# Kernel optimization log

Hardware: AMD Instinct MI355X
Metric: run time of the kernel (lower is better)

## Reference

```python
import jax, jax.numpy as jnp
import numpy as np

N_NODES = 100000
N_EDGES = 1600000
N_FEAT = 128
HIDDEN = 128
N_GRAPHS = 100


def setup_inputs() -> dict:
    key = jax.random.key(0)
    ks = jax.random.split(key, 12)
    glorot = lambda k, fi, fo: jax.random.normal(k, (fo, fi), jnp.float32) * (1.0 / np.sqrt(fi))
    x = jax.random.normal(ks[0], (N_NODES, N_FEAT), jnp.float32)
    edge_index = jax.random.randint(ks[1], (2, N_EDGES), 0, N_NODES, jnp.int64)
    batch = jnp.sort(jax.random.randint(ks[2], (N_NODES,), 0, N_GRAPHS, jnp.int64))
    return {
        "x": x,
        "edge_index": edge_index,
        "batch": batch,
        "W1": glorot(ks[3], N_FEAT, HIDDEN), "b1": jnp.zeros((HIDDEN,), jnp.float32),
        "W2": glorot(ks[4], HIDDEN, HIDDEN), "b2": jnp.zeros((HIDDEN,), jnp.float32),
        "W3": glorot(ks[5], HIDDEN, HIDDEN), "b3": jnp.zeros((HIDDEN,), jnp.float32),
        "W4": glorot(ks[6], HIDDEN, HIDDEN), "b4": jnp.zeros((HIDDEN,), jnp.float32),
    }


def _aggregate(x, edge_index):
    # GIN aggregation with eps=0: (1+eps)*x_i + sum_{j in N(i)} x_j
    src, dst = edge_index[0], edge_index[1]
    agg = jax.ops.segment_sum(x[src], dst, num_segments=N_NODES)
    return x + agg


def _mlp(h, Wa, ba, Wb, bb):
    h = jax.nn.relu(h @ Wa.T + ba)
    return jax.nn.relu(h @ Wb.T + bb)


def reference(x, edge_index, batch, W1, b1, W2, b2, W3, b3, W4, b4):
    # conv1: GINConv(MLP1), then extra relu (no-op after MLP's relu), dropout in eval = identity
    h = _mlp(_aggregate(x, edge_index), W1, b1, W2, b2)
    # conv2: GINConv(MLP2), then relu
    h = _mlp(_aggregate(h, edge_index), W3, b3, W4, b4)
    # global mean pool over graphs
    sums = jax.ops.segment_sum(h, batch, num_segments=N_GRAPHS)
    counts = jax.ops.segment_sum(jnp.ones((h.shape[0],), h.dtype), batch, num_segments=N_GRAPHS)
    x_pool = sums / jnp.maximum(counts, 1.0)[:, None]
    return (x_pool, h)
```

## Files before the change

### kernel.cpp

```cpp
#include <hip/hip_runtime.h>

#define N_NODES  100000
#define N_EDGES  1600000
#define NF       128
#define N_GRAPHS 100
#define NBKT     196
#define BKT_SHIFT 9
#define EPB      4096
#define EB_GRID  391

typedef __attribute__((ext_vector_type(8))) short bf16x8;
typedef __attribute__((ext_vector_type(4))) float f32x4;
typedef unsigned int uint32;

__device__ __forceinline__ unsigned short f2bf(float f) {
    union { float f; uint32 u; } x; x.f = f;
    return (unsigned short)((x.u + 0x7fffu + ((x.u >> 16) & 1u)) >> 16);
}
__device__ __forceinline__ uint32 pack2bf(float a, float b) {
    union { float f; uint32 u; } x, y; x.f = a; y.f = b;
    uint32 lo = (x.u + 0x7fffu + ((x.u >> 16) & 1u)) >> 16;
    uint32 hi = (y.u + 0x7fffu + ((y.u >> 16) & 1u)) & 0xffff0000u;
    return lo | hi;
}

__global__ __launch_bounds__(256) void conv_bf16(const float4* __restrict__ in,
                                                 uint4* __restrict__ out, int n8) {
    int i = blockIdx.x * 256 + threadIdx.x;
    if (i >= n8) return;
    float4 a = in[i * 2], b = in[i * 2 + 1];
    uint4 o;
    o.x = pack2bf(a.x, a.y); o.y = pack2bf(a.z, a.w);
    o.z = pack2bf(b.x, b.y); o.w = pack2bf(b.z, b.w);
    out[i] = o;
}

__global__ __launch_bounds__(256) void conv_w4(const float4* __restrict__ w1,
                                               const float4* __restrict__ w2,
                                               const float4* __restrict__ w3,
                                               const float4* __restrict__ w4,
                                               uint4* __restrict__ out) {
    int i = blockIdx.x * 256 + threadIdx.x;
    int wi = i >> 11, li = i & 2047;
    const float4* src = (wi == 0) ? w1 : (wi == 1) ? w2 : (wi == 2) ? w3 : w4;
    float4 a = src[li * 2], b = src[li * 2 + 1];
    uint4 o;
    o.x = pack2bf(a.x, a.y); o.y = pack2bf(a.z, a.w);
    o.z = pack2bf(b.x, b.y); o.w = pack2bf(b.z, b.w);
    out[i] = o;
}

__global__ __launch_bounds__(256) void bhist(const int* __restrict__ dst,
                                             int* __restrict__ gcnt) {
    __shared__ int h[NBKT];
    int t = threadIdx.x;
    if (t < NBKT) h[t] = 0;
    __syncthreads();
    int e0 = blockIdx.x * EPB;
    #pragma unroll
    for (int i = 0; i < 16; ++i) {
        int e = e0 + i * 256 + t;
        if (e < N_EDGES) atomicAdd(&h[dst[e] >> BKT_SHIFT], 1);
    }
    __syncthreads();
    if (t < NBKT) atomicAdd(&gcnt[t], h[t]);
}

__global__ __launch_bounds__(256) void bscan(const int* __restrict__ gcnt,
                                             int* __restrict__ bbase,
                                             int* __restrict__ cur,
                                             int* __restrict__ rowptr) {
    __shared__ int s[256];
    int t = threadIdx.x;
    int v = (t < NBKT) ? gcnt[t] : 0;
    s[t] = v;
    __syncthreads();
    for (int o = 1; o < 256; o <<= 1) {
        int x = (t >= o) ? s[t - o] : 0;
        __syncthreads();
        s[t] += x;
        __syncthreads();
    }
    if (t < NBKT) { int ex = s[t] - v; bbase[t] = ex; cur[t] = ex; }
    if (t == 0)  { bbase[NBKT] = N_EDGES; rowptr[N_NODES] = N_EDGES; }
}

__global__ __launch_bounds__(256) void bscatter(const int* __restrict__ src,
                                                const int* __restrict__ dst,
                                                int* __restrict__ cur,
                                                uint32* __restrict__ ebuf) {
    __shared__ int lh[NBKT], lbase[NBKT], lcur[NBKT];
    int t = threadIdx.x;
    if (t < NBKT) lh[t] = 0;
    __syncthreads();
    int e0 = blockIdx.x * EPB;
    int d[16];
    #pragma unroll
    for (int i = 0; i < 16; ++i) {
        int e = e0 + i * 256 + t;
        d[i] = -1;
        if (e < N_EDGES) { d[i] = dst[e]; atomicAdd(&lh[d[i] >> BKT_SHIFT], 1); }
    }
    __syncthreads();
    if (t < NBKT) { lbase[t] = atomicAdd(&cur[t], lh[t]); lcur[t] = 0; }
    __syncthreads();
    #pragma unroll
    for (int i = 0; i < 16; ++i) {
        int e = e0 + i * 256 + t;
        if (e < N_EDGES) {
            int b = d[i] >> BKT_SHIFT;
            int off = atomicAdd(&lcur[b], 1);
            ebuf[lbase[b] + off] = ((uint32)(d[i] & 511) << 17) | (uint32)src[e];
        }
    }
}

__global__ __launch_bounds__(256) void bfine(const uint32* __restrict__ ebuf,
                                             const int* __restrict__ bbase,
                                             int* __restrict__ rowptr,
                                             int* __restrict__ csr) {
    __shared__ int deg[512];
    __shared__ int off[512];
    __shared__ int sc[256];
    int t = threadIdx.x;
    int bkt = blockIdx.x;
    int beg = bbase[bkt], end = bbase[bkt + 1];
    deg[t] = 0; deg[t + 256] = 0;
    __syncthreads();
    for (int e = beg + t; e < end; e += 256)
        atomicAdd(&deg[ebuf[e] >> 17], 1);
    __syncthreads();
    int d0 = deg[2 * t], d1 = deg[2 * t + 1];
    sc[t] = d0 + d1;
    __syncthreads();
    for (int o = 1; o < 256; o <<= 1) {
        int x = (t >= o) ? sc[t - o] : 0;
        __syncthreads();
        sc[t] += x;
        __syncthreads();
    }
    int ex = sc[t] - (d0 + d1);
    off[2 * t] = ex; off[2 * t + 1] = ex + d0;
    __syncthreads();
    int node0 = bkt << BKT_SHIFT;
    for (int i = t; i < 512; i += 256) {
        int node = node0 + i;
        if (node < N_NODES) rowptr[node] = beg + off[i];
    }
    __syncthreads();
    for (int e = beg + t; e < end; e += 256) {
        uint32 u = ebuf[e];
        int dl = u >> 17, s = (int)(u & 0x1FFFFu);
        int pos = atomicAdd(&off[dl], 1);
        csr[beg + pos] = s;
    }
}

__global__ __launch_bounds__(256) void gather_agg_bf16(const uint4* __restrict__ x,
                                                       const int* __restrict__ rowptr,
                                                       const int* __restrict__ csr,
                                                       uint4* __restrict__ out) {
    int idx = blockIdx.x * 256 + threadIdx.x;
    int node = idx >> 4, c = idx & 15;
    int beg = rowptr[node], end = rowptr[node + 1];

    float acc[8];
    {
        uint4 v = x[node * 16 + c];
        uint32 u[4] = {v.x, v.y, v.z, v.w};
        #pragma unroll
        for (int i = 0; i < 4; ++i) {
            union { uint32 b; float f; } lo, hi;
            lo.b = u[i] << 16; hi.b = u[i] & 0xffff0000u;
            acc[2 * i] = lo.f; acc[2 * i + 1] = hi.f;
        }
    }
    for (int e = beg; e < end; ++e) {
        int s = csr[e];
        uint4 v = x[s * 16 + c];
        uint32 u[4] = {v.x, v.y, v.z, v.w};
        #pragma unroll
        for (int i = 0; i < 4; ++i) {
            union { uint32 b; float f; } lo, hi;
            lo.b = u[i] << 16; hi.b = u[i] & 0xffff0000u;
            acc[2 * i] += lo.f; acc[2 * i + 1] += hi.f;
        }
    }
    uint4 o;
    o.x = pack2bf(acc[0], acc[1]); o.y = pack2bf(acc[2], acc[3]);
    o.z = pack2bf(acc[4], acc[5]); o.w = pack2bf(acc[6], acc[7]);
    out[node * 16 + c] = o;
}

template <bool F32OUT>
__global__ __launch_bounds__(256) void mlp_mfma(const unsigned short* __restrict__ A,
                                                const unsigned short* __restrict__ Wa,
                                                const float* __restrict__ ba,
                                                const unsigned short* __restrict__ Wb,
                                                const float* __restrict__ bb,
                                                void* __restrict__ Cout, int M) {
    __shared__ unsigned short As[128 * 136];
    __shared__ unsigned short Ws[128 * 136];
    __shared__ float bs1[128], bs2[128];
    int tid  = threadIdx.x;
    int row0 = blockIdx.x * 128;

    #pragma unroll
    for (int it = 0; it < 8; ++it) {
        int li = it * 256 + tid;
        int r = li >> 4, s = li & 15;
        uint4 v = make_uint4(0u, 0u, 0u, 0u);
        if (row0 + r < M) v = *(const uint4*)(A + (size_t)(row0 + r) * NF + s * 8);
        *(uint4*)&As[r * 136 + s * 8] = v;
        *(uint4*)&Ws[r * 136 + s * 8] = *(const uint4*)(Wa + r * NF + s * 8);
    }
    if (tid < 128) { bs1[tid] = ba[tid]; bs2[tid] = bb[tid]; }
    __syncthreads();

    int wv = tid >> 6;
    int l  = tid & 63;
    int lm = l & 15;
    int q  = l >> 4;

    f32x4 acc[2][8];
    #pragma unroll
    for (int i = 0; i < 2; ++i)
        #pragma unroll
        for (int j = 0; j < 8; ++j) acc[i][j] = (f32x4){0.f, 0.f, 0.f, 0.f};

    #pragma unroll
    for (int ks = 0; ks < 4; ++ks) {
        int ko = ks * 32 + q * 8;
        bf16x8 a0 = *(const bf16x8*)&As[(wv * 32 + lm) * 136 + ko];
        bf16x8 a1 = *(const bf16x8*)&As[(wv * 32 + 16 + lm) * 136 + ko];
        #pragma unroll
        for (int ct = 0; ct < 8; ++ct) {
            bf16x8 b = *(const bf16x8*)&Ws[(ct * 16 + lm) * 136 + ko];
            acc[0][ct] = __builtin_amdgcn_mfma_f32_16x16x32_bf16(a0, b, acc[0][ct], 0, 0, 0);
            acc[1][ct] = __builtin_amdgcn_mfma_f32_16x16x32_bf16(a1, b, acc[1][ct], 0, 0, 0);
        }
    }
    __syncthreads();

    #pragma unroll
    for (int rt = 0; rt < 2; ++rt)
        #pragma unroll
        for (int ct = 0; ct < 8; ++ct) {
            int col = ct * 16 + lm;
            float bv = bs1[col];
            #pragma unroll
            for (int r = 0; r < 4; ++r) {
                int rr = wv * 32 + rt * 16 + q * 4 + r;
                As[rr * 136 + col] = f2bf(fmaxf(acc[rt][ct][r] + bv, 0.f));
            }
        }
    #pragma unroll
    for (int it = 0; it < 8; ++it) {
        int li = it * 256 + tid;
        int r = li >> 4, s = li & 15;
        *(uint4*)&Ws[r * 136 + s * 8] = *(const uint4*)(Wb + r * NF + s * 8);
    }
    __syncthreads();

    #pragma unroll
    for (int i = 0; i < 2; ++i)
        #pragma unroll
        for (int j = 0; j < 8; ++j) acc[i][j] = (f32x4){0.f, 0.f, 0.f, 0.f};

    #pragma unroll
    for (int ks = 0; ks < 4; ++ks) {
        int ko = ks * 32 + q * 8;
        bf16x8 a0 = *(const bf16x8*)&As[(wv * 32 + lm) * 136 + ko];
        bf16x8 a1 = *(const bf16x8*)&As[(wv * 32 + 16 + lm) * 136 + ko];
        #pragma unroll
        for (int ct = 0; ct < 8; ++ct) {
            bf16x8 b = *(const bf16x8*)&Ws[(ct * 16 + lm) * 136 + ko];
            acc[0][ct] = __builtin_amdgcn_mfma_f32_16x16x32_bf16(a0, b, acc[0][ct], 0, 0, 0);
            acc[1][ct] = __builtin_amdgcn_mfma_f32_16x16x32_bf16(a1, b, acc[1][ct], 0, 0, 0);
        }
    }

    #pragma unroll
    for (int rt = 0; rt < 2; ++rt)
        #pragma unroll
        for (int ct = 0; ct < 8; ++ct) {
            int col = ct * 16 + lm;
            float bv = bs2[col];
            #pragma unroll
            for (int r = 0; r < 4; ++r) {
                int row = row0 + wv * 32 + rt * 16 + q * 4 + r;
                if (row < M) {
                    float v = fmaxf(acc[rt][ct][r] + bv, 0.f);
                    if (F32OUT) ((float*)Cout)[(size_t)row * NF + col] = v;
                    else ((unsigned short*)Cout)[(size_t)row * NF + col] = f2bf(v);
                }
            }
        }
}

__global__ __launch_bounds__(256) void pool_sum2(const float* __restrict__ h,
                                                 const int* __restrict__ batch,
                                                 float* __restrict__ sums) {
    int t = threadIdx.x;
    int f = t & 127, seg = t >> 7;
    int n0 = blockIdx.x * 128 + seg * 64;
    if (n0 >= N_NODES) return;
    int n1 = min(n0 + 64, N_NODES);
    int cur = batch[n0];
    float acc = 0.f;
    for (int n = n0; n < n1; ++n) {
        int g = batch[n];
        if (g != cur) {
            atomicAdd(&sums[cur * NF + f], acc);
            acc = 0.f; cur = g;
        }
        acc += h[(size_t)n * NF + f];
    }
    atomicAdd(&sums[cur * NF + f], acc);
}

__global__ __launch_bounds__(256) void pool_div2(const float* __restrict__ sums,
                                                 const int* __restrict__ batch,
                                                 float* __restrict__ out) {
    int i = blockIdx.x * 256 + threadIdx.x;
    if (i >= N_GRAPHS * NF) return;
    int g = i >> 7;
    int lo = 0, hi = N_NODES;
    while (lo < hi) { int m = (lo + hi) >> 1; if (batch[m] < g) lo = m + 1; else hi = m; }
    int lo2 = lo, hi2 = N_NODES;
    while (lo2 < hi2) { int m = (lo2 + hi2) >> 1; if (batch[m] < g + 1) lo2 = m + 1; else hi2 = m; }
    float cnt = (float)(lo2 - lo);
    out[i] = sums[i] / fmaxf(cnt, 1.f);
}

extern "C" void kernel_launch(void* const* d_in, const int* in_sizes, int n_in,
                              void* d_out, int out_size, void* d_ws, size_t ws_size,
                              hipStream_t stream) {
    const float* x     = (const float*)d_in[0];
    const int*   ei    = (const int*)d_in[1];
    const int*   batch = (const int*)d_in[2];
    const float* W1 = (const float*)d_in[3];  const float* b1 = (const float*)d_in[4];
    const float* W2 = (const float*)d_in[5];  const float* b2 = (const float*)d_in[6];
    const float* W3 = (const float*)d_in[7];  const float* b3 = (const float*)d_in[8];
    const float* W4 = (const float*)d_in[9];  const float* b4 = (const float*)d_in[10];
    const int* src = ei;
    const int* dst = ei + N_EDGES;

    float* out   = (float*)d_out;
    float* h_out = out + N_GRAPHS * NF;

    const size_t NE = (size_t)N_NODES * NF;
    unsigned short* xb = (unsigned short*)d_ws;
    unsigned short* t0 = xb + NE;
    unsigned short* t1 = t0 + NE;
    unsigned short* Wb = t1 + NE;
    int*    rowptr = (int*)(Wb + 4 * NF * NF);
    int*    csr    = rowptr + N_NODES + 1;
    uint32* ebuf   = (uint32*)(csr + N_EDGES);
    int*    gcnt   = (int*)(ebuf + N_EDGES);
    int*    bbase  = gcnt + NBKT;
    int*    curp   = bbase + NBKT + 1;
    float*  sums   = (float*)(curp + NBKT);

    const int gather_blocks = N_NODES * 16 / 256;
    const int gemm_blocks   = (N_NODES + 127) / 128;

    hipMemsetAsync(gcnt, 0, NBKT * sizeof(int), stream);
    hipMemsetAsync(sums, 0, N_GRAPHS * NF * sizeof(float), stream);

    conv_bf16<<<(int)(NE / 8 + 255) / 256, 256, 0, stream>>>((const float4*)x, (uint4*)xb, (int)(NE / 8));
    conv_w4<<<32, 256, 0, stream>>>((const float4*)W1, (const float4*)W2,
                                    (const float4*)W3, (const float4*)W4, (uint4*)Wb);

    bhist<<<EB_GRID, 256, 0, stream>>>(dst, gcnt);
    bscan<<<1, 256, 0, stream>>>(gcnt, bbase, curp, rowptr);
    bscatter<<<EB_GRID, 256, 0, stream>>>(src, dst, curp, ebuf);
    bfine<<<NBKT, 256, 0, stream>>>(ebuf, bbase, rowptr, csr);

    gather_agg_bf16<<<gather_blocks, 256, 0, stream>>>((const uint4*)xb, rowptr, csr, (uint4*)t0);
    mlp_mfma<false><<<gemm_blocks, 256, 0, stream>>>(t0, Wb + 0 * NF * NF, b1,
                                                     Wb + 1 * NF * NF, b2, t1, N_NODES);

    gather_agg_bf16<<<gather_blocks, 256, 0, stream>>>((const uint4*)t1, rowptr, csr, (uint4*)t0);
    mlp_mfma<true ><<<gemm_blocks, 256, 0, stream>>>(t0, Wb + 2 * NF * NF, b3,
                                                     Wb + 3 * NF * NF, b4, h_out, N_NODES);

    pool_sum2<<<(N_NODES + 127) / 128, 256, 0, stream>>>(h_out, batch, sums);
    pool_div2<<<(N_GRAPHS * NF + 255) / 256, 256, 0, stream>>>(sums, batch, out);
}
```

Baseline: 428.4 us.

## Fuse prep kernels, use fixed-capacity buckets, and load MLP operands directly from global

One prep kernel now converts x and the weights to bf16 and zeroes the counters, replacing two memsets and two conversion launches. The histogram and scan passes are dropped by giving each destination bucket a fixed-capacity slot (CAP) and storing per-node row ends. bfine runs with 512 threads and a single-level scan. The MLP kernel reads A and W fragments straight from global memory instead of staging them in LDS, keeping LDS only for the intermediate activation, with a 4-block occupancy hint. The fixed capacity can overflow if a bucket gets more than CAP edges, and direct global loads may cost more memory traffic than the LDS staging did.

```diff
diff --git a/kernel.cpp b/kernel.cpp
--- a/kernel.cpp
+++ b/kernel.cpp
@@ -6,6 +6,7 @@
 #define N_GRAPHS 100
 #define NBKT     196
 #define BKT_SHIFT 9
+#define CAP      12288
 #define EPB      4096
 #define EB_GRID  391
 
@@ -24,72 +25,42 @@
     return lo | hi;
 }
 
-__global__ __launch_bounds__(256) void conv_bf16(const float4* __restrict__ in,
-                                                 uint4* __restrict__ out, int n8) {
-    int i = blockIdx.x * 256 + threadIdx.x;
-    if (i >= n8) return;
-    float4 a = in[i * 2], b = in[i * 2 + 1];
-    uint4 o;
-    o.x = pack2bf(a.x, a.y); o.y = pack2bf(a.z, a.w);
-    o.z = pack2bf(b.x, b.y); o.w = pack2bf(b.z, b.w);
-    out[i] = o;
-}
-
-__global__ __launch_bounds__(256) void conv_w4(const float4* __restrict__ w1,
-                                               const float4* __restrict__ w2,
-                                               const float4* __restrict__ w3,
-                                               const float4* __restrict__ w4,
-                                               uint4* __restrict__ out) {
-    int i = blockIdx.x * 256 + threadIdx.x;
-    int wi = i >> 11, li = i & 2047;
-    const float4* src = (wi == 0) ? w1 : (wi == 1) ? w2 : (wi == 2) ? w3 : w4;
-    float4 a = src[li * 2], b = src[li * 2 + 1];
-    uint4 o;
-    o.x = pack2bf(a.x, a.y); o.y = pack2bf(a.z, a.w);
-    o.z = pack2bf(b.x, b.y); o.w = pack2bf(b.z, b.w);
-    out[i] = o;
-}
-
-__global__ __launch_bounds__(256) void bhist(const int* __restrict__ dst,
-                                             int* __restrict__ gcnt) {
-    __shared__ int h[NBKT];
-    int t = threadIdx.x;
-    if (t < NBKT) h[t] = 0;
-    __syncthreads();
-    int e0 = blockIdx.x * EPB;
-    #pragma unroll
-    for (int i = 0; i < 16; ++i) {
-        int e = e0 + i * 256 + t;
-        if (e < N_EDGES) atomicAdd(&h[dst[e] >> BKT_SHIFT], 1);
-    }
-    __syncthreads();
-    if (t < NBKT) atomicAdd(&gcnt[t], h[t]);
-}
-
-__global__ __launch_bounds__(256) void bscan(const int* __restrict__ gcnt,
-                                             int* __restrict__ bbase,
-                                             int* __restrict__ cur,
-                                             int* __restrict__ rowptr) {
-    __shared__ int s[256];
-    int t = threadIdx.x;
-    int v = (t < NBKT) ? gcnt[t] : 0;
-    s[t] = v;
-    __syncthreads();
-    for (int o = 1; o < 256; o <<= 1) {
-        int x = (t >= o) ? s[t - o] : 0;
-        __syncthreads();
-        s[t] += x;
-        __syncthreads();
-    }
-    if (t < NBKT) { int ex = s[t] - v; bbase[t] = ex; cur[t] = ex; }
-    if (t == 0)  { bbase[NBKT] = N_EDGES; rowptr[N_NODES] = N_EDGES; }
+__global__ __launch_bounds__(256) void prep(const float4* __restrict__ x,
+                                            const float4* __restrict__ w1,
+                                            const float4* __restrict__ w2,
+                                            const float4* __restrict__ w3,
+                                            const float4* __restrict__ w4,
+                                            uint4* __restrict__ xb, uint4* __restrict__ wb,
+                                            int* __restrict__ cur, float* __restrict__ sums) {
+    int bid = blockIdx.x, t = threadIdx.x;
+    if (bid < 6250) {
+        int i = bid * 256 + t;
+        float4 a = x[i * 2], b = x[i * 2 + 1];
+        uint4 o;
+        o.x = pack2bf(a.x, a.y); o.y = pack2bf(a.z, a.w);
+        o.z = pack2bf(b.x, b.y); o.w = pack2bf(b.z, b.w);
+        xb[i] = o;
+    } else if (bid < 6282) {
+        int i = (bid - 6250) * 256 + t;
+        int wi = i >> 11, li = i & 2047;
+        const float4* s = (wi == 0) ? w1 : (wi == 1) ? w2 : (wi == 2) ? w3 : w4;
+        float4 a = s[li * 2], b = s[li * 2 + 1];
+        uint4 o;
+        o.x = pack2bf(a.x, a.y); o.y = pack2bf(a.z, a.w);
+        o.z = pack2bf(b.x, b.y); o.w = pack2bf(b.z, b.w);
+        wb[i] = o;
+    } else {
+        int idx = (bid - 6282) * 256 + t;
+        for (int i = idx; i < N_GRAPHS * NF; i += 4096) sums[i] = 0.f;
+        if (idx < NBKT) cur[idx] = 0;
+    }
 }
 
 __global__ __launch_bounds__(256) void bscatter(const int* __restrict__ src,
                                                 const int* __restrict__ dst,
                                                 int* __restrict__ cur,
                                                 uint32* __restrict__ ebuf) {
-    __shared__ int lh[NBKT], lbase[NBKT], lcur[NBKT];
+    __shared__ int lh[NBKT], lbase[NBKT];
     int t = threadIdx.x;
     if (t < NBKT) lh[t] = 0;
     __syncthreads();
@@ -102,67 +73,64 @@
         if (e < N_EDGES) { d[i] = dst[e]; atomicAdd(&lh[d[i] >> BKT_SHIFT], 1); }
     }
     __syncthreads();
-    if (t < NBKT) { lbase[t] = atomicAdd(&cur[t], lh[t]); lcur[t] = 0; }
+    if (t < NBKT) { lbase[t] = t * CAP + atomicAdd(&cur[t], lh[t]); lh[t] = 0; }
     __syncthreads();
     #pragma unroll
     for (int i = 0; i < 16; ++i) {
         int e = e0 + i * 256 + t;
         if (e < N_EDGES) {
             int b = d[i] >> BKT_SHIFT;
-            int off = atomicAdd(&lcur[b], 1);
+            int off = atomicAdd(&lh[b], 1);
             ebuf[lbase[b] + off] = ((uint32)(d[i] & 511) << 17) | (uint32)src[e];
         }
     }
 }
 
-__global__ __launch_bounds__(256) void bfine(const uint32* __restrict__ ebuf,
-                                             const int* __restrict__ bbase,
+__global__ __launch_bounds__(512) void bfine(const uint32* __restrict__ ebuf,
+                                             const int* __restrict__ cur,
                                              int* __restrict__ rowptr,
+                                             int* __restrict__ rowend,
                                              int* __restrict__ csr) {
-    __shared__ int deg[512];
-    __shared__ int off[512];
-    __shared__ int sc[256];
+    __shared__ int deg[512], off[512];
     int t = threadIdx.x;
     int bkt = blockIdx.x;
-    int beg = bbase[bkt], end = bbase[bkt + 1];
-    deg[t] = 0; deg[t + 256] = 0;
-    __syncthreads();
-    for (int e = beg + t; e < end; e += 256)
+    int beg = bkt * CAP;
+    int end = beg + cur[bkt];
+    deg[t] = 0;
+    __syncthreads();
+    for (int e = beg + t; e < end; e += 512)
         atomicAdd(&deg[ebuf[e] >> 17], 1);
     __syncthreads();
-    int d0 = deg[2 * t], d1 = deg[2 * t + 1];
-    sc[t] = d0 + d1;
-    __syncthreads();
-    for (int o = 1; o < 256; o <<= 1) {
-        int x = (t >= o) ? sc[t - o] : 0;
+    int d = deg[t];
+    off[t] = d;
+    __syncthreads();
+    for (int o = 1; o < 512; o <<= 1) {
+        int x = (t >= o) ? off[t - o] : 0;
         __syncthreads();
-        sc[t] += x;
+        off[t] += x;
         __syncthreads();
     }
-    int ex = sc[t] - (d0 + d1);
-    off[2 * t] = ex; off[2 * t + 1] = ex + d0;
-    __syncthreads();
-    int node0 = bkt << BKT_SHIFT;
-    for (int i = t; i < 512; i += 256) {
-        int node = node0 + i;
-        if (node < N_NODES) rowptr[node] = beg + off[i];
-    }
-    __syncthreads();
-    for (int e = beg + t; e < end; e += 256) {
+    int ex = off[t] - d;
+    int node = (bkt << BKT_SHIFT) + t;
+    if (node < N_NODES) { rowptr[node] = beg + ex; rowend[node] = beg + ex + d; }
+    __syncthreads();
+    off[t] = ex;
+    __syncthreads();
+    for (int e = beg + t; e < end; e += 512) {
         uint32 u = ebuf[e];
-        int dl = u >> 17, s = (int)(u & 0x1FFFFu);
-        int pos = atomicAdd(&off[dl], 1);
-        csr[beg + pos] = s;
+        int pos = atomicAdd(&off[u >> 17], 1);
+        csr[beg + pos] = (int)(u & 0x1FFFFu);
     }
 }
 
 __global__ __launch_bounds__(256) void gather_agg_bf16(const uint4* __restrict__ x,
                                                        const int* __restrict__ rowptr,
+                                                       const int* __restrict__ rowend,
                                                        const int* __restrict__ csr,
                                                        uint4* __restrict__ out) {
     int idx = blockIdx.x * 256 + threadIdx.x;
     int node = idx >> 4, c = idx & 15;
-    int beg = rowptr[node], end = rowptr[node + 1];
+    int beg = rowptr[node], end = rowend[node];
 
     float acc[8];
     {
@@ -193,34 +161,21 @@
 }
 
 template <bool F32OUT>
-__global__ __launch_bounds__(256) void mlp_mfma(const unsigned short* __restrict__ A,
-                                                const unsigned short* __restrict__ Wa,
-                                                const float* __restrict__ ba,
-                                                const unsigned short* __restrict__ Wb,
-                                                const float* __restrict__ bb,
-                                                void* __restrict__ Cout, int M) {
-    __shared__ unsigned short As[128 * 136];
-    __shared__ unsigned short Ws[128 * 136];
-    __shared__ float bs1[128], bs2[128];
+__global__ __launch_bounds__(256, 4) void mlp_mfma(const unsigned short* __restrict__ A,
+                                                   const unsigned short* __restrict__ Wa,
+                                                   const float* __restrict__ ba,
+                                                   const unsigned short* __restrict__ Wb,
+                                                   const float* __restrict__ bb,
+                                                   void* __restrict__ Cout, int M) {
+    __shared__ unsigned short Mid[128 * 136];
     int tid  = threadIdx.x;
     int row0 = blockIdx.x * 128;
-
-    #pragma unroll
-    for (int it = 0; it < 8; ++it) {
-        int li = it * 256 + tid;
-        int r = li >> 4, s = li & 15;
-        uint4 v = make_uint4(0u, 0u, 0u, 0u);
-        if (row0 + r < M) v = *(const uint4*)(A + (size_t)(row0 + r) * NF + s * 8);
-        *(uint4*)&As[r * 136 + s * 8] = v;
-        *(uint4*)&Ws[r * 136 + s * 8] = *(const uint4*)(Wa + r * NF + s * 8);
-    }
-    if (tid < 128) { bs1[tid] = ba[tid]; bs2[tid] = bb[tid]; }
-    __syncthreads();
-
-    int wv = tid >> 6;
-    int l  = tid & 63;
-    int lm = l & 15;
-    int q  = l >> 4;
+    int wv = tid >> 6, l = tid & 63, lm = l & 15, q = l >> 4;
+
+    const unsigned short* pa0 = A + (size_t)min(row0 + wv * 32 + lm,      M - 1) * NF;
+    const unsigned short* pa1 = A + (size_t)min(row0 + wv * 32 + 16 + lm, M - 1) * NF;
+    const unsigned short* pwa = Wa + lm * NF;
+    const unsigned short* pwb = Wb + lm * NF;
 
     f32x4 acc[2][8];
     #pragma unroll
@@ -231,35 +186,28 @@
     #pragma unroll
     for (int ks = 0; ks < 4; ++ks) {
         int ko = ks * 32 + q * 8;
-        bf16x8 a0 = *(const bf16x8*)&As[(wv * 32 + lm) * 136 + ko];
-        bf16x8 a1 = *(const bf16x8*)&As[(wv * 32 + 16 + lm) * 136 + ko];
+        bf16x8 a0 = *(const bf16x8*)(pa0 + ko);
+        bf16x8 a1 = *(const bf16x8*)(pa1 + ko);
         #pragma unroll
         for (int ct = 0; ct < 8; ++ct) {
-            bf16x8 b = *(const bf16x8*)&Ws[(ct * 16 + lm) * 136 + ko];
+            bf16x8 b = *(const bf16x8*)(pwa + ct * 16 * NF + ko);
             acc[0][ct] = __builtin_amdgcn_mfma_f32_16x16x32_bf16(a0, b, acc[0][ct], 0, 0, 0);
             acc[1][ct] = __builtin_amdgcn_mfma_f32_16x16x32_bf16(a1, b, acc[1][ct], 0, 0, 0);
         }
     }
-    __syncthreads();
 
     #pragma unroll
     for (int rt = 0; rt < 2; ++rt)
         #pragma unroll
         for (int ct = 0; ct < 8; ++ct) {
             int col = ct * 16 + lm;
-            float bv = bs1[col];
+            float bv = ba[col];
             #pragma unroll
             for (int r = 0; r < 4; ++r) {
                 int rr = wv * 32 + rt * 16 + q * 4 + r;
-                As[rr * 136 + col] = f2bf(fmaxf(acc[rt][ct][r] + bv, 0.f));
+                Mid[rr * 136 + col] = f2bf(fmaxf(acc[rt][ct][r] + bv, 0.f));
             }
         }
-    #pragma unroll
-    for (int it = 0; it < 8; ++it) {
-        int li = it * 256 + tid;
-        int r = li >> 4, s = li & 15;
-        *(uint4*)&Ws[r * 136 + s * 8] = *(const uint4*)(Wb + r * NF + s * 8);
-    }
     __syncthreads();
 
     #pragma unroll
@@ -267,14 +215,16 @@
         #pragma unroll
         for (int j = 0; j < 8; ++j) acc[i][j] = (f32x4){0.f, 0.f, 0.f, 0.f};
 
+    const unsigned short* pm0 = &Mid[(wv * 32 + lm) * 136];
+    const unsigned short* pm1 = &Mid[(wv * 32 + 16 + lm) * 136];
     #pragma unroll
     for (int ks = 0; ks < 4; ++ks) {
         int ko = ks * 32 + q * 8;
-        bf16x8 a0 = *(const bf16x8*)&As[(wv * 32 + lm) * 136 + ko];
-        bf16x8 a1 = *(const bf16x8*)&As[(wv * 32 + 16 + lm) * 136 + ko];
+        bf16x8 a0 = *(const bf16x8*)(pm0 + ko);
+        bf16x8 a1 = *(const bf16x8*)(pm1 + ko);
         #pragma unroll
         for (int ct = 0; ct < 8; ++ct) {
-            bf16x8 b = *(const bf16x8*)&Ws[(ct * 16 + lm) * 136 + ko];
+            bf16x8 b = *(const bf16x8*)(pwb + ct * 16 * NF + ko);
             acc[0][ct] = __builtin_amdgcn_mfma_f32_16x16x32_bf16(a0, b, acc[0][ct], 0, 0, 0);
             acc[1][ct] = __builtin_amdgcn_mfma_f32_16x16x32_bf16(a1, b, acc[1][ct], 0, 0, 0);
         }
@@ -285,7 +235,7 @@
         #pragma unroll
         for (int ct = 0; ct < 8; ++ct) {
             int col = ct * 16 + lm;
-            float bv = bs2[col];
+            float bv = bb[col];
             #pragma unroll
             for (int r = 0; r < 4; ++r) {
                 int row = row0 + wv * 32 + rt * 16 + q * 4 + r;
@@ -355,33 +305,28 @@
     unsigned short* t1 = t0 + NE;
     unsigned short* Wb = t1 + NE;
     int*    rowptr = (int*)(Wb + 4 * NF * NF);
-    int*    csr    = rowptr + N_NODES + 1;
-    uint32* ebuf   = (uint32*)(csr + N_EDGES);
-    int*    gcnt   = (int*)(ebuf + N_EDGES);
-    int*    bbase  = gcnt + NBKT;
-    int*    curp   = bbase + NBKT + 1;
+    int*    rowend = rowptr + N_NODES;
+    int*    csr    = rowend + N_NODES;
+    uint32* ebuf   = (uint32*)(csr + NBKT * CAP);
+    int*    curp   = (int*)(ebuf + NBKT * CAP);
     float*  sums   = (float*)(curp + NBKT);
 
     const int gather_blocks = N_NODES * 16 / 256;
     const int gemm_blocks   = (N_NODES + 127) / 128;
 
-    hipMemsetAsync(gcnt, 0, NBKT * sizeof(int), stream);
-    hipMemsetAsync(sums, 0, N_GRAPHS * NF * sizeof(float), stream);
-
-    conv_bf16<<<(int)(NE / 8 + 255) / 256, 256, 0, stream>>>((const float4*)x, (uint4*)xb, (int)(NE / 8));
-    conv_w4<<<32, 256, 0, stream>>>((const float4*)W1, (const float4*)W2,
-                                    (const float4*)W3, (const float4*)W4, (uint4*)Wb);
-
-    bhist<<<EB_GRID, 256, 0, stream>>>(dst, gcnt);
-    bscan<<<1, 256, 0, stream>>>(gcnt, bbase, curp, rowptr);
+    prep<<<6250 + 32 + 16, 256, 0, stream>>>((const float4*)x,
+                                             (const float4*)W1, (const float4*)W2,
+                                             (const float4*)W3, (const float4*)W4,
+                                             (uint4*)xb, (uint4*)Wb, curp, sums);
+
     bscatter<<<EB_GRID, 256, 0, stream>>>(src, dst, curp, ebuf);
-    bfine<<<NBKT, 256, 0, stream>>>(ebuf, bbase, rowptr, csr);
-
-    gather_agg_bf16<<<gather_blocks, 256, 0, stream>>>((const uint4*)xb, rowptr, csr, (uint4*)t0);
+    bfine<<<NBKT, 512, 0, stream>>>(ebuf, curp, rowptr, rowend, csr);
+
+    gather_agg_bf16<<<gather_blocks, 256, 0, stream>>>((const uint4*)xb, rowptr, rowend, csr, (uint4*)t0);
     mlp_mfma<false><<<gemm_blocks, 256, 0, stream>>>(t0, Wb + 0 * NF * NF, b1,
                                                      Wb + 1 * NF * NF, b2, t1, N_NODES);
 
-    gather_agg_bf16<<<gather_blocks, 256, 0, stream>>>((const uint4*)t1, rowptr, csr, (uint4*)t0);
+    gather_agg_bf16<<<gather_blocks, 256, 0, stream>>>((const uint4*)t1, rowptr, rowend, csr, (uint4*)t0);
     mlp_mfma<true ><<<gemm_blocks, 256, 0, stream>>>(t0, Wb + 2 * NF * NF, b3,
                                                      Wb + 3 * NF * NF, b4, h_out, N_NODES);
 
```

Result: no change. 430.6 us (+0.5%).
